# Performance work log

Hardware: AMD Instinct MI355X
Metric: run time of the kernel (lower is better)

Reference implementation:

```python
import jax, jax.numpy as jnp
import numpy as np

B, N, D, K, H, HID, ITERS = 16, 4096, 64, 8, 4, 256, 3
DH = D // H
EPS = 1e-5


def _ln(x, g, b):
    m = x.mean(-1, keepdims=True)
    v = x.var(-1, keepdims=True)
    return (x - m) / jnp.sqrt(v + EPS) * g + b


def setup_inputs() -> dict:
    ks = jax.random.split(jax.random.key(0), 16)
    s = 1.0 / np.sqrt(D)
    return {
        "embeddings": jax.random.normal(ks[0], (B, N, D), dtype=jnp.float32),
        "slots_mu": jax.random.normal(ks[1], (1, K, D), dtype=jnp.float32) * 0.1,
        "slots_logsigma": jax.random.normal(ks[2], (1, K, D), dtype=jnp.float32) * 0.1,
        "mixing_init": jnp.full((1, K), 1.0 / K, dtype=jnp.float32),
        "to_keys": jax.random.uniform(ks[3], (K, D, D), dtype=jnp.float32),
        "to_queries": jax.random.uniform(ks[4], (K, D, D), dtype=jnp.float32),
        "to_values": jax.random.uniform(ks[5], (K, D, D), dtype=jnp.float32),
        "w_ih": jax.random.uniform(ks[6], (3 * D, D), minval=-s, maxval=s),
        "w_hh": jax.random.uniform(ks[7], (3 * D, D), minval=-s, maxval=s),
        "b_ih": jax.random.uniform(ks[8], (3 * D,), minval=-s, maxval=s),
        "b_hh": jax.random.uniform(ks[9], (3 * D,), minval=-s, maxval=s),
        "w1": jax.random.uniform(ks[10], (HID, D), minval=-s, maxval=s),
        "b1": jnp.zeros((HID,), jnp.float32),
        "w2": jax.random.uniform(ks[11], (D, HID), minval=-1.0 / np.sqrt(HID), maxval=1.0 / np.sqrt(HID)),
        "b2": jnp.zeros((D,), jnp.float32),
        "ln_in_g": jnp.ones((D,), jnp.float32), "ln_in_b": jnp.zeros((D,), jnp.float32),
        "ln_sl_g": jnp.ones((D,), jnp.float32), "ln_sl_b": jnp.zeros((D,), jnp.float32),
        "ln_ff_g": jnp.ones((D,), jnp.float32), "ln_ff_b": jnp.zeros((D,), jnp.float32),
        "noise_init": jax.random.normal(ks[12], (B, K, D), dtype=jnp.float32),
        "noise_final": jax.random.normal(ks[13], (B, K, D), dtype=jnp.float32),
    }


def reference(embeddings, slots_mu, slots_logsigma, mixing_init, to_keys, to_queries,
              to_values, w_ih, w_hh, b_ih, b_hh, w1, b1, w2, b2,
              ln_in_g, ln_in_b, ln_sl_g, ln_sl_b, ln_ff_g, ln_ff_b,
              noise_init, noise_final):
    mu = jnp.broadcast_to(slots_mu, (B, K, D))
    sigma = jnp.broadcast_to(jnp.exp(slots_logsigma), (B, K, D))
    slots = mu + sigma * noise_init                              # [B,K,D]
    mixing = jnp.broadcast_to(mixing_init, (B, K))[:, :, None]   # [B,K,1]

    x = _ln(embeddings, ln_in_g, ln_in_b)                        # [B,N,D]
    keys = jnp.einsum('bne,ked->bknd', x, to_keys).reshape(B, K, N, H, DH)
    values = jnp.einsum('bne,ked->bknd', x, to_values).reshape(B, K, N, H, DH)
    sigma = sigma.reshape(B, K, H, DH)
    # torch.einsum('bkd,kdd->bkd') uses the DIAGONAL of to_queries
    qdiag = jnp.einsum('kdd->kd', to_queries)                    # [K,D]
    log_pi = -0.5 * D * np.log(2.0 * np.pi)

    attn_vis = None
    for _ in range(ITERS):
        slots_prev = slots
        s_ln = _ln(slots, ln_sl_g, ln_sl_b)
        queries = (s_ln * qdiag[None]).reshape(B, K, H, DH)      # [B,K,H,Dh]
        exponent = -0.5 * (keys - queries[:, :, None]) ** 2 / (sigma[:, :, None] ** 2 + EPS)
        log_scale = -jnp.log(jnp.clip(sigma, EPS, None))[:, :, None]  # [B,K,1,H,Dh]
        gll = jnp.log(mixing + EPS)[..., None] + (log_pi + log_scale + exponent).sum(-1)  # [B,K,N,H]
        attn = jax.nn.softmax(gll, axis=1) + EPS
        attn_vis = attn
        Nk = attn.sum(axis=(2, 3))[:, :, None]                   # [B,K,1]
        upd = jnp.einsum('bknh,bknhd->bkhd', attn, values).reshape(B, K, D)
        upd = (1.0 / Nk + EPS) * upd
        nq = upd.reshape(B, K, H, DH)                            # source overwrites new_queries with slot_updates
        sig2 = jnp.einsum('bknh,bknhd->bkhd', attn, (keys - nq[:, :, None]) ** 2).reshape(B, K, D)
        sigma = (jnp.sqrt(sig2 / Nk) + EPS).reshape(B, K, H, DH)
        mixing = Nk / N
        # GRUCell (torch gate order: reset, update, new)
        xg = upd.reshape(-1, D) @ w_ih.T + b_ih
        hg = slots_prev.reshape(-1, D) @ w_hh.T + b_hh
        xr, xz, xn = jnp.split(xg, 3, axis=-1)
        hr, hz, hn = jnp.split(hg, 3, axis=-1)
        r = jax.nn.sigmoid(xr + hr)
        z = jax.nn.sigmoid(xz + hz)
        n = jnp.tanh(xn + r * hn)
        slots = ((1.0 - z) * n + z * slots_prev.reshape(-1, D)).reshape(B, K, D)
        pre = _ln(slots, ln_ff_g, ln_ff_b)
        slots = slots + jax.nn.relu(pre @ w1.T + b1) @ w2.T + b2

    sigma = sigma.reshape(B, K, D)
    slots = slots + sigma * noise_final
    return slots, attn_vis
```

## Files before the change

kernel.cpp:

```cpp
#include <hip/hip_runtime.h>
#include <math.h>

#define B_ 16
#define N_ 4096
#define D_ 64
#define K_ 8
#define H_ 4
#define HID_ 256
#define ITERS_ 3
#define EPS_ 1e-5f

#define HTERM_ (-940.9930580015849f)

__device__ __forceinline__ float waveReduceSum64(float v) {
  v += __shfl_xor(v, 1);  v += __shfl_xor(v, 2);  v += __shfl_xor(v, 4);
  v += __shfl_xor(v, 8);  v += __shfl_xor(v, 16); v += __shfl_xor(v, 32);
  return v;
}
__device__ __forceinline__ float groupReduceSum16(float v) {
  v += __shfl_xor(v, 1); v += __shfl_xor(v, 2); v += __shfl_xor(v, 4);
  v += __shfl_xor(v, 8);
  return v;
}

template <int CTRL>
__device__ __forceinline__ float dpp_mov(float v) {
  return __int_as_float(__builtin_amdgcn_update_dpp(
      0, __float_as_int(v), CTRL, 0xF, 0xF, true));
}
__device__ __forceinline__ float row16Sum(float v) {
  v += dpp_mov<0xB1>(v);
  v += dpp_mov<0x4E>(v);
  v += dpp_mov<0x124>(v);
  v += dpp_mov<0x128>(v);
  return v;
}

__global__ void ln_emb_kernel(const float* __restrict__ emb,
                              const float* __restrict__ g, const float* __restrict__ b,
                              float* __restrict__ x, int b0) {
  int wave = threadIdx.x >> 6, lane = threadIdx.x & 63;
  int row = blockIdx.x * 4 + wave;
  float e = emb[((size_t)b0 * N_ + row) * 64 + lane];
  float s  = waveReduceSum64(e);
  float sq = waveReduceSum64(e * e);
  float mean = s * (1.0f / 64.0f);
  float var  = sq * (1.0f / 64.0f) - mean * mean;
  float inv  = rsqrtf(var + EPS_);
  x[(size_t)row * 64 + lane] = (e - mean) * inv * g[lane] + b[lane];
}

__global__ __launch_bounds__(256) void key_kernel(const float* __restrict__ x,
    const float* __restrict__ Wk, float* __restrict__ keys) {
  __shared__ float xs[64 * 65];
  __shared__ float wks[64 * 64];
  int n0 = blockIdx.x * 64;
  int k  = blockIdx.y;
  int bl = blockIdx.z;
  int tid = threadIdx.x;

  const float* xb = x + ((size_t)bl * N_ + n0) * 64;
  for (int i = tid; i < 4096; i += 256)
    xs[(i >> 6) * 65 + (i & 63)] = xb[i];
  const float4* wk4 = (const float4*)(Wk + (size_t)k * 4096);
  float4* wks4 = (float4*)wks;
  for (int i = tid; i < 1024; i += 256) wks4[i] = wk4[i];
  __syncthreads();

  int tr = tid >> 4, tc = tid & 15;
  int r0 = tr * 4, c0 = tc * 4;
  float ak[4][4] = {{0.f}};
  #pragma unroll 4
  for (int kk = 0; kk < 64; ++kk) {
    float xv[4];
    #pragma unroll
    for (int i = 0; i < 4; ++i) xv[i] = xs[(r0 + i) * 65 + kk];
    float4 wkq = *(const float4*)&wks[kk * 64 + c0];
    float wkc[4] = {wkq.x, wkq.y, wkq.z, wkq.w};
    #pragma unroll
    for (int i = 0; i < 4; ++i)
      #pragma unroll
      for (int j = 0; j < 4; ++j)
        ak[i][j] = fmaf(xv[i], wkc[j], ak[i][j]);
  }
  size_t outb = ((size_t)bl * N_ + n0) * 512 + (size_t)k * 64;
  #pragma unroll
  for (int i = 0; i < 4; ++i) {
    float4 kq = make_float4(ak[i][0], ak[i][1], ak[i][2], ak[i][3]);
    *(float4*)&keys[outb + (size_t)(r0 + i) * 512 + c0] = kq;
  }
}

__global__ void init_kernel(const float* __restrict__ mu, const float* __restrict__ lsig,
                            const float* __restrict__ mix0, const float* __restrict__ noise,
                            float* __restrict__ slots, float* __restrict__ sigma,
                            float* __restrict__ mixing, int b0) {
  int g = b0 * 512 + blockIdx.x * 256 + threadIdx.x;
  int kd = g & 511;
  float sg = expf(lsig[kd]);
  slots[g] = mu[kd] + sg * noise[g];
  sigma[g] = sg;
  if ((g & 63) == 0) mixing[g >> 6] = mix0[(g >> 6) & (K_ - 1)];
}

__global__ void prep_kernel(const float* __restrict__ slots, const float* __restrict__ sigma,
                            const float* __restrict__ mixing, const float* __restrict__ tq,
                            const float* __restrict__ g_sl, const float* __restrict__ b_sl,
                            float* __restrict__ q, float* __restrict__ i2s,
                            float* __restrict__ base, float* __restrict__ S1,
                            float* __restrict__ S2, float* __restrict__ S0,
                            float* __restrict__ T, int b0) {
  int bk = b0 * K_ + blockIdx.x;
  int lane = threadIdx.x;
  int k = bk & (K_ - 1);
  float s  = slots[bk * 64 + lane];
  float su = waveReduceSum64(s);
  float sq = waveReduceSum64(s * s);
  float mean = su * (1.0f / 64.0f);
  float var  = sq * (1.0f / 64.0f) - mean * mean;
  float sl = (s - mean) * rsqrtf(var + EPS_) * g_sl[lane] + b_sl[lane];
  q[bk * 64 + lane] = sl * tq[k * 4096 + lane * 65];
  float sg = sigma[bk * 64 + lane];
  i2s[bk * 64 + lane] = 0.5f / (sg * sg + EPS_);
  float ls = -logf(fmaxf(sg, EPS_));
  float lss = groupReduceSum16(ls);
  if ((lane & 15) == 0)
    base[bk * 4 + (lane >> 4)] = logf(mixing[bk] + EPS_) + HTERM_ + lss;
  S1[bk * 64 + lane] = 0.0f;
  S2[bk * 64 + lane] = 0.0f;
  T[bk * 256 + lane]       = 0.0f;
  T[bk * 256 + 64 + lane]  = 0.0f;
  T[bk * 256 + 128 + lane] = 0.0f;
  T[bk * 256 + 192 + lane] = 0.0f;
  if (lane < 4) S0[bk * 4 + lane] = 0.0f;
}

template <bool WRITE_ATTN>
__global__ __launch_bounds__(256, 4) void attn_kernel(
    const float* __restrict__ keys, const float* __restrict__ x,
    const float* __restrict__ q, const float* __restrict__ i2s, const float* __restrict__ base,
    float* __restrict__ S1, float* __restrict__ S2, float* __restrict__ S0,
    float* __restrict__ T, float* __restrict__ attn_out, int b0) {
  int bl = blockIdx.y;
  int bg = b0 + bl;
  int wave = threadIdx.x >> 6, lane = threadIdx.x & 63;
  int h = lane >> 4;
  int n0 = (blockIdx.x * 4 + wave) * 16;

  __shared__ float att_lds[4][K_][64];
  __shared__ float blk[3104];
  __shared__ float bv_lds[32];
  for (int i = threadIdx.x; i < 3104; i += 256) blk[i] = 0.0f;
  if (threadIdx.x < 32) bv_lds[threadIdx.x] = base[bg * 32 + threadIdx.x];

  float qv[K_], iv[K_];
  {
    const float* qp = q + bg * 512 + lane;
    const float* ip = i2s + bg * 512 + lane;
    #pragma unroll
    for (int k = 0; k < K_; ++k) { qv[k] = qp[k * 64]; iv[k] = ip[k * 64]; }
  }
  float s1a[K_] = {0.f}, s2a[K_] = {0.f};
  __syncthreads();

  const float* kptr = keys + ((size_t)bl * N_ + n0) * 512 + lane;
  #pragma unroll 2
  for (int ni = 0; ni < 16; ++ni) {
    float key[K_], gl[K_];
    #pragma unroll
    for (int k = 0; k < K_; ++k) key[k] = kptr[k * 64];
    #pragma unroll
    for (int k = 0; k < K_; ++k) {
      float df = key[k] - qv[k];
      float t = row16Sum(df * df * iv[k]);
      gl[k] = bv_lds[k * 4 + h] - t;
    }
    float m = gl[0];
    #pragma unroll
    for (int k = 1; k < K_; ++k) m = fmaxf(m, gl[k]);
    float ssum = 0.f;
    #pragma unroll
    for (int k = 0; k < K_; ++k) { gl[k] = __expf(gl[k] - m); ssum += gl[k]; }
    float inv = __builtin_amdgcn_rcpf(ssum);
    #pragma unroll
    for (int k = 0; k < K_; ++k) {
      float a = gl[k] * inv + EPS_;
      s1a[k] = fmaf(a, key[k], s1a[k]);
      s2a[k] = fmaf(a * key[k], key[k], s2a[k]);
      if ((lane & 15) == 0) att_lds[wave][k][ni * 4 + h] = a;
    }
    kptr += 512;
  }
  #pragma unroll
  for (int k = 0; k < K_; ++k) {
    atomicAdd(&blk[k * 64 + lane],       s1a[k]);
    atomicAdd(&blk[512 + k * 64 + lane], s2a[k]);
  }

  float xr[16];
  {
    const float* xptr = x + ((size_t)bl * N_ + n0) * 64 + lane;
    #pragma unroll
    for (int ni = 0; ni < 16; ++ni) xr[ni] = xptr[ni * 64];
  }
  #pragma unroll
  for (int k = 0; k < K_; ++k) {
    float t0 = 0.f, t1 = 0.f, t2 = 0.f, t3 = 0.f;
    float c0 = 0.f, c1 = 0.f, c2 = 0.f, c3 = 0.f;
    #pragma unroll
    for (int ni = 0; ni < 16; ++ni) {
      float4 a4 = *(const float4*)&att_lds[wave][k][ni * 4];
      float xv = xr[ni];
      t0 = fmaf(a4.x, xv, t0); t1 = fmaf(a4.y, xv, t1);
      t2 = fmaf(a4.z, xv, t2); t3 = fmaf(a4.w, xv, t3);
      c0 += a4.x; c1 += a4.y; c2 += a4.z; c3 += a4.w;
    }
    atomicAdd(&blk[1024 + k * 256 + lane],       t0);
    atomicAdd(&blk[1024 + k * 256 + 64 + lane],  t1);
    atomicAdd(&blk[1024 + k * 256 + 128 + lane], t2);
    atomicAdd(&blk[1024 + k * 256 + 192 + lane], t3);
    if (lane == 0) {
      atomicAdd(&blk[3072 + k * 4 + 0], c0);
      atomicAdd(&blk[3072 + k * 4 + 1], c1);
      atomicAdd(&blk[3072 + k * 4 + 2], c2);
      atomicAdd(&blk[3072 + k * 4 + 3], c3);
    }
  }
  __syncthreads();
  for (int i = threadIdx.x; i < 512; i += 256) {
    atomicAdd(&S1[bg * 512 + i], blk[i]);
    atomicAdd(&S2[bg * 512 + i], blk[512 + i]);
  }
  for (int i = threadIdx.x; i < 2048; i += 256)
    atomicAdd(&T[bg * 2048 + i], blk[1024 + i]);
  if (threadIdx.x < 32) atomicAdd(&S0[bg * 32 + threadIdx.x], blk[3072 + threadIdx.x]);
  if (WRITE_ATTN) {
    #pragma unroll
    for (int k = 0; k < K_; ++k)
      attn_out[((size_t)(bg * K_ + k) * N_ + n0) * 4 + lane] = att_lds[wave][k][lane];
  }
}

__global__ __launch_bounds__(256) void update_kernel(
    const float* __restrict__ S1, const float* __restrict__ S2,
    const float* __restrict__ S0, const float* __restrict__ T,
    const float* __restrict__ Wv,
    float* __restrict__ slots, float* __restrict__ sigma, float* __restrict__ mixing,
    const float* __restrict__ w_ih, const float* __restrict__ w_hh,
    const float* __restrict__ b_ih, const float* __restrict__ b_hh,
    const float* __restrict__ w1, const float* __restrict__ b1,
    const float* __restrict__ w2, const float* __restrict__ b2,
    const float* __restrict__ g_ff, const float* __restrict__ b_ff,
    const float* __restrict__ noise_final, float* __restrict__ out_slots,
    int last, int b0) {
  int bk = b0 * K_ + blockIdx.x;
  int k = bk & (K_ - 1);
  int t = threadIdx.x;
  __shared__ float upd_s[64], sp_s[64], sig_s[64], xg_s[192], hg_s[192],
                   snew_s[64], pre_s[64], hid_s[256];
  if (t < 64) {
    float nk = S0[bk * 4 + 0] + S0[bk * 4 + 1] + S0[bk * 4 + 2] + S0[bk * 4 + 3];
    float sv = 0.f;
    const float* Trow = T + bk * 256 + (t >> 4) * 64;
    const float* wv = Wv + (size_t)k * 4096 + t;
    #pragma unroll 8
    for (int e = 0; e < 64; ++e) sv = fmaf(Trow[e], wv[(size_t)e * 64], sv);
    float upd = (1.0f / nk + EPS_) * sv;
    upd_s[t] = upd;
    float s1 = S1[bk * 64 + t], s2 = S2[bk * 64 + t], s0 = S0[bk * 4 + (t >> 4)];
    float sig2 = fmaxf(s2 - 2.0f * upd * s1 + upd * upd * s0, 0.0f);
    float sg = sqrtf(sig2 / nk) + EPS_;
    sigma[bk * 64 + t] = sg;
    sig_s[t] = sg;
    sp_s[t] = slots[bk * 64 + t];
    if (t == 0) mixing[bk] = nk / (float)N_;
  }
  __syncthreads();
  if (t < 192) {
    const float4* wr = (const float4*)(w_ih + t * 64);
    const float4* wh = (const float4*)(w_hh + t * 64);
    float a1 = b_ih[t], a2 = b_hh[t];
    #pragma unroll
    for (int d4 = 0; d4 < 16; ++d4) {
      float4 wa = wr[d4], wb = wh[d4];
      const float* u  = &upd_s[d4 * 4];
      const float* sp = &sp_s[d4 * 4];
      a1 += u[0] * wa.x + u[1] * wa.y + u[2] * wa.z + u[3] * wa.w;
      a2 += sp[0] * wb.x + sp[1] * wb.y + sp[2] * wb.z + sp[3] * wb.w;
    }
    xg_s[t] = a1;
    hg_s[t] = a2;
  }
  __syncthreads();
  if (t < 64) {
    float r = 1.0f / (1.0f + expf(-(xg_s[t] + hg_s[t])));
    float z = 1.0f / (1.0f + expf(-(xg_s[64 + t] + hg_s[64 + t])));
    float nn = tanhf(xg_s[128 + t] + r * hg_s[128 + t]);
    float sn = (1.0f - z) * nn + z * sp_s[t];
    snew_s[t] = sn;
    float su = waveReduceSum64(sn);
    float sq = waveReduceSum64(sn * sn);
    float mean = su * (1.0f / 64.0f);
    float var  = sq * (1.0f / 64.0f) - mean * mean;
    pre_s[t] = (sn - mean) * rsqrtf(var + EPS_) * g_ff[t] + b_ff[t];
  }
  __syncthreads();
  {
    const float4* w1r = (const float4*)(w1 + t * 64);
    float a = b1[t];
    #pragma unroll
    for (int d4 = 0; d4 < 16; ++d4) {
      float4 w = w1r[d4];
      const float* p = &pre_s[d4 * 4];
      a += p[0] * w.x + p[1] * w.y + p[2] * w.z + p[3] * w.w;
    }
    hid_s[t] = fmaxf(a, 0.0f);
  }
  __syncthreads();
  if (t < 64) {
    const float4* w2r = (const float4*)(w2 + t * 256);
    float a = b2[t];
    #pragma unroll
    for (int j4 = 0; j4 < 64; ++j4) {
      float4 w = w2r[j4];
      const float* p = &hid_s[j4 * 4];
      a += p[0] * w.x + p[1] * w.y + p[2] * w.z + p[3] * w.w;
    }
    float outv = snew_s[t] + a;
    slots[bk * 64 + t] = outv;
    if (last) out_slots[bk * 64 + t] = outv + sig_s[t] * noise_final[bk * 64 + t];
  }
}

extern "C" void kernel_launch(void* const* d_in, const int* in_sizes, int n_in,
                              void* d_out, int out_size, void* d_ws, size_t ws_size,
                              hipStream_t stream) {
  const float* emb  = (const float*)d_in[0];
  const float* mu   = (const float*)d_in[1];
  const float* lsig = (const float*)d_in[2];
  const float* mix0 = (const float*)d_in[3];
  const float* Wk   = (const float*)d_in[4];
  const float* Wq   = (const float*)d_in[5];
  const float* Wv   = (const float*)d_in[6];
  const float* w_ih = (const float*)d_in[7];
  const float* w_hh = (const float*)d_in[8];
  const float* b_ih = (const float*)d_in[9];
  const float* b_hh = (const float*)d_in[10];
  const float* w1   = (const float*)d_in[11];
  const float* b1   = (const float*)d_in[12];
  const float* w2   = (const float*)d_in[13];
  const float* b2   = (const float*)d_in[14];
  const float* g_in = (const float*)d_in[15];
  const float* b_in = (const float*)d_in[16];
  const float* g_sl = (const float*)d_in[17];
  const float* b_sl = (const float*)d_in[18];
  const float* g_ff = (const float*)d_in[19];
  const float* b_ff = (const float*)d_in[20];
  const float* nz0  = (const float*)d_in[21];
  const float* nzf  = (const float*)d_in[22];

  float* ws = (float*)d_ws;
  float* slots  = ws;
  float* sigma  = slots + 8192;
  float* q      = sigma + 8192;
  float* i2s    = q + 8192;
  float* S1     = i2s + 8192;
  float* S2     = S1 + 8192;
  float* S0     = S2 + 8192;
  float* base   = S0 + 512;
  float* mixing = base + 512;
  float* T      = mixing + 128;
  float* x      = T + 32768;
  const size_t small_bytes = (size_t)(6 * 8192 + 512 + 512 + 128 + 32768) * 4;

  int C = 16;
  while (C > 1 && small_bytes + (size_t)C * 9437184ull > ws_size) C >>= 1;
  float* keys = x + (size_t)C * N_ * 64;

  float* out_slots = (float*)d_out;
  float* out_attn  = out_slots + B_ * K_ * 64;

  for (int b0 = 0; b0 < B_; b0 += C) {
    ln_emb_kernel<<<dim3(C * N_ / 4), 256, 0, stream>>>(emb, g_in, b_in, x, b0);
    key_kernel<<<dim3(N_ / 64, K_, C), 256, 0, stream>>>(x, Wk, keys);
    init_kernel<<<dim3(C * 2), 256, 0, stream>>>(mu, lsig, mix0, nz0, slots, sigma, mixing, b0);
    for (int it = 0; it < ITERS_; ++it) {
      prep_kernel<<<dim3(C * K_), 64, 0, stream>>>(slots, sigma, mixing, Wq, g_sl, b_sl,
                                                   q, i2s, base, S1, S2, S0, T, b0);
      if (it == ITERS_ - 1)
        attn_kernel<true><<<dim3(N_ / 64, C), 256, 0, stream>>>(keys, x, q, i2s, base,
                                                                S1, S2, S0, T, out_attn, b0);
      else
        attn_kernel<false><<<dim3(N_ / 64, C), 256, 0, stream>>>(keys, x, q, i2s, base,
                                                                 S1, S2, S0, T, nullptr, b0);
      update_kernel<<<dim3(C * K_), 256, 0, stream>>>(S1, S2, S0, T, Wv, slots, sigma, mixing,
          w_ih, w_hh, b_ih, b_hh, w1, b1, w2, b2, g_ff, b_ff, nzf, out_slots,
          it == ITERS_ - 1 ? 1 : 0, b0);
    }
  }
}
```

Before: 494.0 us.

## Replace global atomic accumulation with per-block partials reduced in update kernel

Each attention block now writes its LDS-accumulated statistics (S1, S2, T, S0) to a dedicated partials slot instead of issuing global atomicAdds. The update kernel sums the 64 per-block partials for its batch and slot, and the prep kernel no longer zeroes the accumulators. This removes contention on global atomics and the zeroing pass. In exchange it adds workspace per batch and a strided 64-way reduction inside the small update kernel.

```diff
diff --git a/kernel.cpp b/kernel.cpp
--- a/kernel.cpp
+++ b/kernel.cpp
@@ -9,6 +9,7 @@
 #define HID_ 256
 #define ITERS_ 3
 #define EPS_ 1e-5f
+#define PSTRIDE_ 3104
 
 #define HTERM_ (-940.9930580015849f)
 
@@ -107,9 +108,7 @@
                             const float* __restrict__ mixing, const float* __restrict__ tq,
                             const float* __restrict__ g_sl, const float* __restrict__ b_sl,
                             float* __restrict__ q, float* __restrict__ i2s,
-                            float* __restrict__ base, float* __restrict__ S1,
-                            float* __restrict__ S2, float* __restrict__ S0,
-                            float* __restrict__ T, int b0) {
+                            float* __restrict__ base, int b0) {
   int bk = b0 * K_ + blockIdx.x;
   int lane = threadIdx.x;
   int k = bk & (K_ - 1);
@@ -126,21 +125,13 @@
   float lss = groupReduceSum16(ls);
   if ((lane & 15) == 0)
     base[bk * 4 + (lane >> 4)] = logf(mixing[bk] + EPS_) + HTERM_ + lss;
-  S1[bk * 64 + lane] = 0.0f;
-  S2[bk * 64 + lane] = 0.0f;
-  T[bk * 256 + lane]       = 0.0f;
-  T[bk * 256 + 64 + lane]  = 0.0f;
-  T[bk * 256 + 128 + lane] = 0.0f;
-  T[bk * 256 + 192 + lane] = 0.0f;
-  if (lane < 4) S0[bk * 4 + lane] = 0.0f;
 }
 
 template <bool WRITE_ATTN>
 __global__ __launch_bounds__(256, 4) void attn_kernel(
     const float* __restrict__ keys, const float* __restrict__ x,
     const float* __restrict__ q, const float* __restrict__ i2s, const float* __restrict__ base,
-    float* __restrict__ S1, float* __restrict__ S2, float* __restrict__ S0,
-    float* __restrict__ T, float* __restrict__ attn_out, int b0) {
+    float* __restrict__ partials, float* __restrict__ attn_out, int b0) {
   int bl = blockIdx.y;
   int bg = b0 + bl;
   int wave = threadIdx.x >> 6, lane = threadIdx.x & 63;
@@ -148,9 +139,9 @@
   int n0 = (blockIdx.x * 4 + wave) * 16;
 
   __shared__ float att_lds[4][K_][64];
-  __shared__ float blk[3104];
+  __shared__ float blk[PSTRIDE_];
   __shared__ float bv_lds[32];
-  for (int i = threadIdx.x; i < 3104; i += 256) blk[i] = 0.0f;
+  for (int i = threadIdx.x; i < PSTRIDE_; i += 256) blk[i] = 0.0f;
   if (threadIdx.x < 32) bv_lds[threadIdx.x] = base[bg * 32 + threadIdx.x];
 
   float qv[K_], iv[K_];
@@ -227,13 +218,10 @@
     }
   }
   __syncthreads();
-  for (int i = threadIdx.x; i < 512; i += 256) {
-    atomicAdd(&S1[bg * 512 + i], blk[i]);
-    atomicAdd(&S2[bg * 512 + i], blk[512 + i]);
-  }
-  for (int i = threadIdx.x; i < 2048; i += 256)
-    atomicAdd(&T[bg * 2048 + i], blk[1024 + i]);
-  if (threadIdx.x < 32) atomicAdd(&S0[bg * 32 + threadIdx.x], blk[3072 + threadIdx.x]);
+  {
+    float* p = partials + ((size_t)bl * 64 + blockIdx.x) * PSTRIDE_;
+    for (int i = threadIdx.x; i < PSTRIDE_; i += 256) p[i] = blk[i];
+  }
   if (WRITE_ATTN) {
     #pragma unroll
     for (int k = 0; k < K_; ++k)
@@ -242,9 +230,7 @@
 }
 
 __global__ __launch_bounds__(256) void update_kernel(
-    const float* __restrict__ S1, const float* __restrict__ S2,
-    const float* __restrict__ S0, const float* __restrict__ T,
-    const float* __restrict__ Wv,
+    const float* __restrict__ partials, const float* __restrict__ Wv,
     float* __restrict__ slots, float* __restrict__ sigma, float* __restrict__ mixing,
     const float* __restrict__ w_ih, const float* __restrict__ w_hh,
     const float* __restrict__ b_ih, const float* __restrict__ b_hh,
@@ -254,20 +240,43 @@
     const float* __restrict__ noise_final, float* __restrict__ out_slots,
     int last, int b0) {
   int bk = b0 * K_ + blockIdx.x;
-  int k = bk & (K_ - 1);
+  int k = blockIdx.x & (K_ - 1);
+  int bl = blockIdx.x >> 3;
   int t = threadIdx.x;
+  __shared__ float S1l[64], S2l[64], S0l[4], Tl[256];
   __shared__ float upd_s[64], sp_s[64], sig_s[64], xg_s[192], hg_s[192],
                    snew_s[64], pre_s[64], hid_s[256];
+  const float* P = partials + (size_t)bl * 64 * PSTRIDE_;
+  {
+    const float* p = P + 1024 + k * 256 + t;
+    float acc = 0.f;
+    #pragma unroll 8
+    for (int j = 0; j < 64; ++j) acc += p[(size_t)j * PSTRIDE_];
+    Tl[t] = acc;
+  }
+  if (t < 132) {
+    const float* p2;
+    if (t < 64)       p2 = P + k * 64 + t;
+    else if (t < 128) p2 = P + 512 + k * 64 + (t - 64);
+    else              p2 = P + 3072 + k * 4 + (t - 128);
+    float acc = 0.f;
+    #pragma unroll 8
+    for (int j = 0; j < 64; ++j) acc += p2[(size_t)j * PSTRIDE_];
+    if (t < 64) S1l[t] = acc;
+    else if (t < 128) S2l[t - 64] = acc;
+    else S0l[t - 128] = acc;
+  }
+  __syncthreads();
   if (t < 64) {
-    float nk = S0[bk * 4 + 0] + S0[bk * 4 + 1] + S0[bk * 4 + 2] + S0[bk * 4 + 3];
+    float nk = S0l[0] + S0l[1] + S0l[2] + S0l[3];
     float sv = 0.f;
-    const float* Trow = T + bk * 256 + (t >> 4) * 64;
+    const float* Trow = &Tl[(t >> 4) * 64];
     const float* wv = Wv + (size_t)k * 4096 + t;
     #pragma unroll 8
     for (int e = 0; e < 64; ++e) sv = fmaf(Trow[e], wv[(size_t)e * 64], sv);
     float upd = (1.0f / nk + EPS_) * sv;
     upd_s[t] = upd;
-    float s1 = S1[bk * 64 + t], s2 = S2[bk * 64 + t], s0 = S0[bk * 4 + (t >> 4)];
+    float s1 = S1l[t], s2 = S2l[t], s0 = S0l[t >> 4];
     float sig2 = fmaxf(s2 - 2.0f * upd * s1 + upd * upd * s0, 0.0f);
     float sg = sqrtf(sig2 / nk) + EPS_;
     sigma[bk * 64 + t] = sg;
@@ -364,17 +373,16 @@
   float* sigma  = slots + 8192;
   float* q      = sigma + 8192;
   float* i2s    = q + 8192;
-  float* S1     = i2s + 8192;
-  float* S2     = S1 + 8192;
-  float* S0     = S2 + 8192;
-  float* base   = S0 + 512;
+  float* base   = i2s + 8192;
   float* mixing = base + 512;
-  float* T      = mixing + 128;
-  float* x      = T + 32768;
-  const size_t small_bytes = (size_t)(6 * 8192 + 512 + 512 + 128 + 32768) * 4;
+  float* partials = mixing + 128;
+  const size_t small_bytes = (size_t)(4 * 8192 + 512 + 128) * 4;
+  const size_t per_b = (size_t)64 * PSTRIDE_ * 4 + (size_t)N_ * 64 * 4
+                     + (size_t)K_ * N_ * 64 * 4;
 
   int C = 16;
-  while (C > 1 && small_bytes + (size_t)C * 9437184ull > ws_size) C >>= 1;
+  while (C > 1 && small_bytes + (size_t)C * per_b > ws_size) C >>= 1;
+  float* x    = partials + (size_t)64 * C * PSTRIDE_;
   float* keys = x + (size_t)C * N_ * 64;
 
   float* out_slots = (float*)d_out;
@@ -386,14 +394,14 @@
     init_kernel<<<dim3(C * 2), 256, 0, stream>>>(mu, lsig, mix0, nz0, slots, sigma, mixing, b0);
     for (int it = 0; it < ITERS_; ++it) {
       prep_kernel<<<dim3(C * K_), 64, 0, stream>>>(slots, sigma, mixing, Wq, g_sl, b_sl,
-                                                   q, i2s, base, S1, S2, S0, T, b0);
+                                                   q, i2s, base, b0);
       if (it == ITERS_ - 1)
         attn_kernel<true><<<dim3(N_ / 64, C), 256, 0, stream>>>(keys, x, q, i2s, base,
-                                                                S1, S2, S0, T, out_attn, b0);
+                                                                partials, out_attn, b0);
       else
         attn_kernel<false><<<dim3(N_ / 64, C), 256, 0, stream>>>(keys, x, q, i2s, base,
-                                                                 S1, S2, S0, T, nullptr, b0);
-      update_kernel<<<dim3(C * K_), 256, 0, stream>>>(S1, S2, S0, T, Wv, slots, sigma, mixing,
+                                                                 partials, nullptr, b0);
+      update_kernel<<<dim3(C * K_), 256, 0, stream>>>(partials, Wv, slots, sigma, mixing,
           w_ih, w_hh, b_ih, b_hh, w1, b1, w2, b2, g_ff, b_ff, nzf, out_slots,
           it == ITERS_ - 1 ? 1 : 0, b0);
     }
```

Measured after the change: 513.4 us. +3.9%, slower.
